# Kernel tuning notes

Hardware: AMD Instinct MI355X
Metric: run time of the kernel (lower is better)

Reference implementation:

```python
import jax, jax.numpy as jnp
import numpy as np

DIM = 1536
HEADS = 12
HEAD_DIM = 128
SEQ = 3120
FRAME = 1560
EPS = 1e-6


def _rmsnorm(x, gamma, eps=EPS):
    var = jnp.mean(jnp.square(x), axis=-1, keepdims=True)
    return x * jax.lax.rsqrt(var + eps) * gamma


def _rope(x, cos, sin):
    # x: [B,S,H,D], cos/sin: [S, D//2]; rotate interleaved pairs (Wan-style)
    xr = x.reshape(x.shape[:-1] + (x.shape[-1] // 2, 2))
    x1, x2 = xr[..., 0], xr[..., 1]
    c = cos[None, :, None, :]
    s = sin[None, :, None, :]
    o1 = x1 * c - x2 * s
    o2 = x1 * s + x2 * c
    return jnp.stack([o1, o2], axis=-1).reshape(x.shape)


def setup_inputs() -> dict:
    key = jax.random.key(0)
    ks = jax.random.split(key, 8)
    pos = jnp.arange(SEQ, dtype=jnp.float32)[:, None]
    inv_freq = 1.0 / (10000.0 ** (jnp.arange(0, HEAD_DIM // 2, dtype=jnp.float32) / (HEAD_DIM // 2)))
    ang = pos * inv_freq[None, :]
    return {
        "hidden_states": jax.random.normal(ks[0], (1, SEQ, DIM), jnp.float32),
        "freqs_cos": jnp.cos(ang),
        "freqs_sin": jnp.sin(ang),
        "w_qkv": jax.random.normal(ks[1], (DIM, 3 * DIM), jnp.float32) * (DIM ** -0.5),
        "b_qkv": jnp.zeros((3 * DIM,), jnp.float32),
        "g_q": jnp.ones((DIM,), jnp.float32),
        "g_k": jnp.ones((DIM,), jnp.float32),
        "w_out": jax.random.normal(ks[2], (DIM, DIM), jnp.float32) * (DIM ** -0.5),
        "b_out": jnp.zeros((DIM,), jnp.float32),
        "frame_len": FRAME,
    }


def reference(hidden_states, freqs_cos, freqs_sin, w_qkv, b_qkv, g_q, g_k, w_out, b_out, frame_len):
    B, S, _ = hidden_states.shape
    qkv = hidden_states @ w_qkv + b_qkv  # [B,S,3*DIM]
    q, k, v = jnp.split(qkv, 3, axis=-1)
    q = _rmsnorm(q, g_q)
    k = _rmsnorm(k, g_k)
    q = q.reshape(B, S, HEADS, HEAD_DIM)
    k = k.reshape(B, S, HEADS, HEAD_DIM)
    v = v.reshape(B, S, HEADS, HEAD_DIM)
    q = _rope(q, freqs_cos, freqs_sin)
    k = _rope(k, freqs_cos, freqs_sin)
    # block-wise causal mask over frames of frame_len tokens
    blk = jnp.arange(S) // frame_len
    mask = blk[None, :] <= blk[:, None]  # [Sq, Sk]
    scale = 1.0 / jnp.sqrt(jnp.float32(HEAD_DIM))
    scores = jnp.einsum("bqhd,bkhd->bhqk", q, k) * scale
    scores = jnp.where(mask[None, None], scores, jnp.float32(-1e30))
    probs = jax.nn.softmax(scores, axis=-1)
    out = jnp.einsum("bhqk,bkhd->bqhd", probs, v)
    out = out.reshape(B, S, HEADS * HEAD_DIM)
    return out @ w_out + b_out
```

## Files before the change

### kernel.cpp

```cpp
#include <hip/hip_runtime.h>
#include <hip/hip_bf16.h>
#include <stdint.h>

#define SEQ_LEN 3120
#define DIM 1536
#define QKV_N 4608
#define HEADS 12
#define HEAD_DIM 128
#define FRAME_LEN 1560
#define SM_SCALE 0.08838834764831845f
#define LOG2E 1.4426950408889634f
#define FMAXC2 43.280851226669165f
#define BQ 256

#if __has_builtin(__builtin_amdgcn_exp2f)
#define FEXP2(x) __builtin_amdgcn_exp2f(x)
#else
#define FEXP2(x) exp2f(x)
#endif

typedef short short8 __attribute__((ext_vector_type(8)));
typedef float f32x4 __attribute__((ext_vector_type(4)));
typedef float f32x16 __attribute__((ext_vector_type(16)));

__device__ __forceinline__ unsigned short f2bf(float x) {
    union { float f; unsigned u; } v; v.f = x;
    unsigned r = v.u + 0x7fffu + ((v.u >> 16) & 1u);
    return (unsigned short)(r >> 16);
}
__device__ __forceinline__ float bf2f(unsigned short b) {
    union { unsigned u; float f; } v; v.u = ((unsigned)b) << 16;
    return v.f;
}
__device__ __forceinline__ unsigned pk2bf(float a, float b) {
    __hip_bfloat162 h = __float22bfloat162_rn(make_float2(a, b));
    union { __hip_bfloat162 h2; unsigned u; } v; v.h2 = h;
    return v.u;
}

__device__ __forceinline__ void async16(void* lds, const void* g) {
    __builtin_amdgcn_global_load_lds(
        (const __attribute__((address_space(1))) unsigned int*)g,
        (__attribute__((address_space(3))) unsigned int*)lds, 16, 0, 0);
}

__device__ __forceinline__ void transpose_tile(
    const float* __restrict__ in, unsigned short* __restrict__ out,
    int R, int C, int c0, int r0, float (*T)[65], int tid)
{
    const int rl = tid >> 4, cl = (tid & 15) * 4;
#pragma unroll
    for (int i = 0; i < 4; ++i) {
        const int row = r0 + rl + i * 16;
        float4 v = *(const float4*)&in[(size_t)row * C + c0 + cl];
        T[cl + 0][rl + i * 16] = v.x; T[cl + 1][rl + i * 16] = v.y;
        T[cl + 2][rl + i * 16] = v.z; T[cl + 3][rl + i * 16] = v.w;
    }
    __syncthreads();
    const int oc = tid >> 2, ob = (tid & 3) * 16;
    union { unsigned short t[16]; uint4 u[2]; } p;
#pragma unroll
    for (int j = 0; j < 16; ++j) p.t[j] = f2bf(T[oc][ob + j]);
    uint4* dst = (uint4*)&out[(size_t)(c0 + oc) * R + r0 + ob];
    dst[0] = p.u[0];
    dst[1] = p.u[1];
}

__global__ __launch_bounds__(256) void prep_kernel(
    const float* __restrict__ hs, unsigned short* __restrict__ hsb,
    const float* __restrict__ w_qkv, unsigned short* __restrict__ wqkvT,
    const float* __restrict__ w_out, unsigned short* __restrict__ woutT)
{
    __shared__ float T[64][65];
    const int bid = blockIdx.x;
    const int tid = threadIdx.x;
    if (bid < 2340) {
        const int i = bid * 256 + tid;
        const float4 a = ((const float4*)hs)[i * 2];
        const float4 b = ((const float4*)hs)[i * 2 + 1];
        union { unsigned short t[8]; uint4 u; } p;
        p.t[0] = f2bf(a.x); p.t[1] = f2bf(a.y); p.t[2] = f2bf(a.z); p.t[3] = f2bf(a.w);
        p.t[4] = f2bf(b.x); p.t[5] = f2bf(b.y); p.t[6] = f2bf(b.z); p.t[7] = f2bf(b.w);
        ((uint4*)hsb)[i] = p.u;
    } else if (bid < 4068) {
        const int t = bid - 2340;
        transpose_tile(w_qkv, wqkvT, DIM, QKV_N, (t % 72) * 64, (t / 72) * 64, T, tid);
    } else {
        const int t = bid - 4068;
        transpose_tile(w_out, woutT, DIM, DIM, (t % 24) * 64, (t / 24) * 64, T, tid);
    }
}

__global__ __launch_bounds__(256, 2) void gemm_bt_kernel(
    const unsigned short* __restrict__ A, const unsigned short* __restrict__ Bt,
    const float* __restrict__ bias, float* __restrict__ C, int M, int N, int K,
    int ntp, int spx)
{
    __shared__ short As[2][4096];
    __shared__ short Bs[2][4096];

    const int xcd = blockIdx.x & 7;
    const int idx = (xcd & 1) * spx + (blockIdx.x >> 3);
    const int mtiles = (M + 127) >> 7;
    if (idx >= ntp * mtiles) return;
    const int m0 = (idx / ntp) * 128;
    const int n0 = ((xcd >> 1) * ntp + idx % ntp) * 128;

    const int tid = threadIdx.x;
    const int w = tid >> 6, l = tid & 63;
    const int wr = w >> 1, wc = w & 1;
    const int lhi = l >> 4, llo = l & 15;

    f32x4 acc[4][4];
#pragma unroll
    for (int i = 0; i < 4; ++i)
#pragma unroll
        for (int j = 0; j < 4; ++j) acc[i][j] = f32x4{0.f, 0.f, 0.f, 0.f};

    const int c0i = (w * 2) * 64 + l, c1i = c0i + 64;
    const unsigned short* gA0 = A + (size_t)min(m0 + (c0i >> 2), M - 1) * K + (c0i & 3) * 8;
    const unsigned short* gA1 = A + (size_t)min(m0 + (c1i >> 2), M - 1) * K + (c1i & 3) * 8;
    const unsigned short* gB0 = Bt + (size_t)(n0 + (c0i >> 2)) * K + (c0i & 3) * 8;
    const unsigned short* gB1 = Bt + (size_t)(n0 + (c1i >> 2)) * K + (c1i & 3) * 8;

    const int aoff = (wr * 64 + llo) * 32 + lhi * 8;
    const int boff = (wc * 64 + llo) * 32 + lhi * 8;

    auto stage = [&](int k0, int b) {
        async16(As[b] + (w * 2 + 0) * 512, gA0 + k0);
        async16(As[b] + (w * 2 + 1) * 512, gA1 + k0);
        async16(Bs[b] + (w * 2 + 0) * 512, gB0 + k0);
        async16(Bs[b] + (w * 2 + 1) * 512, gB1 + k0);
    };

    const int nk = K >> 5;
    stage(0, 0);
    for (int t = 0; t < nk; ++t) {
        __syncthreads();
        if (t + 1 < nk) stage((t + 1) * 32, (t + 1) & 1);
        const short* A_ = As[t & 1];
        const short* B_ = Bs[t & 1];
        short8 af[4], bf[4];
#pragma unroll
        for (int mt = 0; mt < 4; ++mt) af[mt] = *(const short8*)&A_[aoff + mt * 512];
#pragma unroll
        for (int nt = 0; nt < 4; ++nt) bf[nt] = *(const short8*)&B_[boff + nt * 512];
#pragma unroll
        for (int mt = 0; mt < 4; ++mt)
#pragma unroll
            for (int nt = 0; nt < 4; ++nt)
                acc[mt][nt] = __builtin_amdgcn_mfma_f32_16x16x32_bf16(af[mt], bf[nt], acc[mt][nt], 0, 0, 0);
    }

#pragma unroll
    for (int mt = 0; mt < 4; ++mt)
#pragma unroll
        for (int ri = 0; ri < 4; ++ri) {
            const int row = m0 + wr * 64 + mt * 16 + lhi * 4 + ri;
            if (row < M) {
#pragma unroll
                for (int nt = 0; nt < 4; ++nt) {
                    const int col = n0 + wc * 64 + nt * 16 + llo;
                    C[(size_t)row * N + col] = acc[mt][nt][ri] + bias[col];
                }
            }
        }
}

__global__ __launch_bounds__(256, 2) void gemm_bt_bf16_kernel(
    const unsigned short* __restrict__ A, const unsigned short* __restrict__ Bt,
    const float* __restrict__ bias, unsigned short* __restrict__ C, int M, int N, int K,
    int ntp, int spx)
{
    __shared__ short As[2][4096];
    __shared__ short Bs[2][4096];

    const int xcd = blockIdx.x & 7;
    const int idx = (xcd & 1) * spx + (blockIdx.x >> 3);
    const int mtiles = (M + 127) >> 7;
    if (idx >= ntp * mtiles) return;
    const int m0 = (idx / ntp) * 128;
    const int n0 = ((xcd >> 1) * ntp + idx % ntp) * 128;

    const int tid = threadIdx.x;
    const int w = tid >> 6, l = tid & 63;
    const int wr = w >> 1, wc = w & 1;
    const int lhi = l >> 4, llo = l & 15;

    f32x4 acc[4][4];
#pragma unroll
    for (int i = 0; i < 4; ++i)
#pragma unroll
        for (int j = 0; j < 4; ++j) acc[i][j] = f32x4{0.f, 0.f, 0.f, 0.f};

    const int c0i = (w * 2) * 64 + l, c1i = c0i + 64;
    const unsigned short* gA0 = A + (size_t)min(m0 + (c0i >> 2), M - 1) * K + (c0i & 3) * 8;
    const unsigned short* gA1 = A + (size_t)min(m0 + (c1i >> 2), M - 1) * K + (c1i & 3) * 8;
    const unsigned short* gB0 = Bt + (size_t)(n0 + (c0i >> 2)) * K + (c0i & 3) * 8;
    const unsigned short* gB1 = Bt + (size_t)(n0 + (c1i >> 2)) * K + (c1i & 3) * 8;

    const int aoff = (wr * 64 + llo) * 32 + lhi * 8;
    const int boff = (wc * 64 + llo) * 32 + lhi * 8;

    auto stage = [&](int k0, int b) {
        async16(As[b] + (w * 2 + 0) * 512, gA0 + k0);
        async16(As[b] + (w * 2 + 1) * 512, gA1 + k0);
        async16(Bs[b] + (w * 2 + 0) * 512, gB0 + k0);
        async16(Bs[b] + (w * 2 + 1) * 512, gB1 + k0);
    };

    const int nk = K >> 5;
    stage(0, 0);
    for (int t = 0; t < nk; ++t) {
        __syncthreads();
        if (t + 1 < nk) stage((t + 1) * 32, (t + 1) & 1);
        const short* A_ = As[t & 1];
        const short* B_ = Bs[t & 1];
        short8 af[4], bf[4];
#pragma unroll
        for (int mt = 0; mt < 4; ++mt) af[mt] = *(const short8*)&A_[aoff + mt * 512];
#pragma unroll
        for (int nt = 0; nt < 4; ++nt) bf[nt] = *(const short8*)&B_[boff + nt * 512];
#pragma unroll
        for (int mt = 0; mt < 4; ++mt)
#pragma unroll
            for (int nt = 0; nt < 4; ++nt)
                acc[mt][nt] = __builtin_amdgcn_mfma_f32_16x16x32_bf16(af[mt], bf[nt], acc[mt][nt], 0, 0, 0);
    }

#pragma unroll
    for (int mt = 0; mt < 4; ++mt)
#pragma unroll
        for (int ri = 0; ri < 4; ++ri) {
            const int row = m0 + wr * 64 + mt * 16 + lhi * 4 + ri;
            if (row < M) {
#pragma unroll
                for (int nt = 0; nt < 4; ++nt) {
                    const int col = n0 + wc * 64 + nt * 16 + llo;
                    C[(size_t)row * N + col] = f2bf(acc[mt][nt][ri] + bias[col]);
                }
            }
        }
}

__global__ __launch_bounds__(256) void rmsrope_kernel(
    const unsigned short* __restrict__ qkvb, const float* __restrict__ gq,
    const float* __restrict__ gk, const float* __restrict__ cosf,
    const float* __restrict__ sinf, unsigned short* __restrict__ qb,
    unsigned short* __restrict__ kb)
{
    const int s = blockIdx.x;
    const int tid = threadIdx.x;
    const unsigned short* qrow = qkvb + (size_t)s * QKV_N;
    const unsigned short* krow = qrow + DIM;

    float2 qp[3], kp[3];
    float ssq_q = 0.f, ssq_k = 0.f;
#pragma unroll
    for (int j = 0; j < 3; ++j) {
        const int p = tid + j * 256;
        const unsigned uq = *(const unsigned*)(qrow + 2 * p);
        const unsigned uk = *(const unsigned*)(krow + 2 * p);
        qp[j] = make_float2(bf2f((unsigned short)(uq & 0xffff)), bf2f((unsigned short)(uq >> 16)));
        kp[j] = make_float2(bf2f((unsigned short)(uk & 0xffff)), bf2f((unsigned short)(uk >> 16)));
        ssq_q += qp[j].x * qp[j].x + qp[j].y * qp[j].y;
        ssq_k += kp[j].x * kp[j].x + kp[j].y * kp[j].y;
    }
#pragma unroll
    for (int off = 32; off > 0; off >>= 1) {
        ssq_q += __shfl_down(ssq_q, off);
        ssq_k += __shfl_down(ssq_k, off);
    }
    __shared__ float wq[4], wk[4];
    const int wave = tid >> 6, lane = tid & 63;
    if (lane == 0) { wq[wave] = ssq_q; wk[wave] = ssq_k; }
    __syncthreads();
    const float tq = wq[0] + wq[1] + wq[2] + wq[3];
    const float tk = wk[0] + wk[1] + wk[2] + wk[3];
    const float inv_q = rsqrtf(tq * (1.0f / DIM) + 1e-6f) * (SM_SCALE * LOG2E);
    const float inv_k = rsqrtf(tk * (1.0f / DIM) + 1e-6f);

#pragma unroll
    for (int j = 0; j < 3; ++j) {
        const int p = tid + j * 256;
        const int fi = p & 63;
        const float c = cosf[s * 64 + fi];
        const float si = sinf[s * 64 + fi];
        {
            const float y1 = qp[j].x * inv_q * gq[2 * p];
            const float y2 = qp[j].y * inv_q * gq[2 * p + 1];
            *(unsigned*)&qb[(size_t)s * DIM + 2 * p] = pk2bf(y1 * c - y2 * si, y1 * si + y2 * c);
        }
        {
            const float y1 = kp[j].x * inv_k * gk[2 * p];
            const float y2 = kp[j].y * inv_k * gk[2 * p + 1];
            *(unsigned*)&kb[(size_t)s * DIM + 2 * p] = pk2bf(y1 * c - y2 * si, y1 * si + y2 * c);
        }
    }
}

__global__ __launch_bounds__(256) void vtrans_kernel(
    const unsigned short* __restrict__ qkvb, unsigned short* __restrict__ vt)
{
    __shared__ float T[128][65];
    const int s0 = blockIdx.x * 64;
    const int h = blockIdx.y;
    const int tid = threadIdx.x;
    const int rl = tid >> 2, cb = (tid & 3) * 32;
    const int row = min(s0 + rl, SEQ_LEN - 1);
#pragma unroll
    for (int i = 0; i < 4; ++i) {
        const int d = cb + i * 8;
        union { uint4 u; unsigned short t[8]; } v;
        v.u = *(const uint4*)&qkvb[(size_t)row * QKV_N + 2 * DIM + h * HEAD_DIM + d];
#pragma unroll
        for (int j = 0; j < 8; ++j) T[d + j][rl] = bf2f(v.t[j]);
    }
    __syncthreads();
    const int od = tid >> 1, ob = (tid & 1) * 32;
    const size_t orow = (size_t)(h * HEAD_DIM + od) * SEQ_LEN;
#pragma unroll
    for (int v8 = 0; v8 < 4; ++v8) {
        const int s = s0 + ob + v8 * 8;
        if (s < SEQ_LEN) {
            union { unsigned short t[8]; uint4 u; } pk;
#pragma unroll
            for (int j = 0; j < 8; ++j) pk.t[j] = f2bf(T[od][ob + v8 * 8 + j]);
            *(uint4*)&vt[orow + s] = pk.u;
        }
    }
}

__global__ __launch_bounds__(512, 2) void attn_part_kernel(
    const unsigned short* __restrict__ qb, const unsigned short* __restrict__ kb,
    const unsigned short* __restrict__ vt, unsigned short* __restrict__ part_o,
    float* __restrict__ part_ml)
{
    __shared__ short KV[40960];

    const int bid = blockIdx.x;
    const int xcd = bid & 7;
    const int slot = bid >> 3;
    int h, bx;
    if (slot < 20) { h = xcd; bx = slot; }
    else { h = 8 + (xcd >> 1); bx = (xcd & 1) * 10 + (slot - 20); }

    const int tid = threadIdx.x;
    const int w = tid >> 6;
    const int l = tid & 63;
    int tile, split, nsp;
    if (bx < 6) { tile = bx; split = 0; nsp = 1; }
    else { const int b2 = bx - 6; tile = 6 + (b2 >> 1); split = b2 & 1; nsp = 2; }
    const int q0 = tile * BQ;
    const int lhi = l >> 5;
    const int llo = l & 31;

#pragma unroll
    for (int s = 0; s < 8; ++s) {
        const int c = (s * 8 + w) * 64 + l;
        const int row = c >> 4, g = c & 15;
        const int gr = min(q0 + row, SEQ_LEN - 1);
        async16(KV + (s * 8 + w) * 512, qb + (size_t)gr * DIM + h * HEAD_DIM + g * 8);
    }
    __syncthreads();
    short8 qf[8];
#pragma unroll
    for (int ds = 0; ds < 8; ++ds)
        qf[ds] = *(const short8*)&KV[(w * 32 + llo) * 128 + ds * 16 + lhi * 8];
    __syncthreads();

    const int myq = q0 + w * 32 + llo;
    const int mylimit = (myq < FRAME_LEN) ? FRAME_LEN : SEQ_LEN;
    const int wave_lim = (q0 + w * 32 < FRAME_LEN) ? FRAME_LEN : SEQ_LEN;
    const int Lmax = (tile < 6) ? FRAME_LEN : SEQ_LEN;
    const int nch = (Lmax + 63) >> 6;
    const int kc0 = ((split * nch) / nsp) * 64;
    const int kc1 = (((split + 1) * nch) / nsp) * 64;
    const int nchunks = (kc1 - kc0) >> 6;

    float l_run = 0.f;
    f32x16 o[4];
#pragma unroll
    for (int mt = 0; mt < 4; ++mt)
#pragma unroll
        for (int r = 0; r < 16; ++r) o[mt][r] = 0.f;

    int krloc[2], kcol[2], vcol[2], lof[2];
    size_t vrow[2];
#pragma unroll
    for (int s = 0; s < 2; ++s) {
        const int c = (s * 8 + w) * 64 + l;
        const int kr = c >> 4;
        krloc[s] = kr;
        kcol[s] = h * HEAD_DIM + (((c & 15) ^ (kr & 7)) * 8);
        const int d = c >> 3;
        vrow[s] = (size_t)(h * HEAD_DIM + d) * SEQ_LEN;
        vcol[s] = ((c & 7) ^ (d & 7)) * 8;
        lof[s] = (s * 8 + w) * 512;
    }

    auto issueK = [&](int kc, int b) {
#pragma unroll
        for (int s = 0; s < 2; ++s) {
            const int gr = min(kc + krloc[s], SEQ_LEN - 1);
            async16(KV + b * 8192 + lof[s], kb + (size_t)gr * DIM + kcol[s]);
        }
    };
    auto issueV = [&](int kc, int t) {
#pragma unroll
        for (int s = 0; s < 2; ++s) {
            const int col = min(kc + vcol[s], SEQ_LEN - 8);
            async16(KV + 16384 + t * 8192 + lof[s], vt + vrow[s] + col);
        }
    };

    auto qkt = [&](f32x16* st, int b) {
        const short* Kb = KV + b * 8192;
#pragma unroll
        for (int r = 0; r < 16; ++r) { st[0][r] = 0.f; st[1][r] = 0.f; }
#pragma unroll
        for (int ds = 0; ds < 8; ++ds) {
            const int gd = ds * 2 + lhi;
#pragma unroll
            for (int kt = 0; kt < 2; ++kt) {
                const int krow = kt * 32 + llo;
                short8 kf = *(const short8*)&Kb[krow * 128 + ((gd ^ (krow & 7)) * 8)];
                st[kt] = __builtin_amdgcn_mfma_f32_32x32x16_bf16(kf, qf[ds], st[kt], 0, 0, 0);
            }
        }
    };

    auto sm_pv = [&](f32x16* st, int kc, int t) {
        if (kc + 64 > wave_lim) {
#pragma unroll
            for (int kt = 0; kt < 2; ++kt)
#pragma unroll
                for (int r = 0; r < 16; ++r) {
                    const int kg = kc + kt * 32 + (r & 3) + 8 * (r >> 2) + 4 * lhi;
                    if (kg >= mylimit) st[kt][r] = -3.0e38f;
                }
        }
        float rs = 0.f;
        unsigned p16[2][8];
#pragma unroll
        for (int kt = 0; kt < 2; ++kt)
#pragma unroll
            for (int r2 = 0; r2 < 8; ++r2) {
                const float p0 = FEXP2(st[kt][2 * r2] - FMAXC2);
                const float p1 = FEXP2(st[kt][2 * r2 + 1] - FMAXC2);
                rs += p0 + p1;
                p16[kt][r2] = pk2bf(p0, p1);
            }
        l_run += rs;

        const short* Vb = KV + 16384 + t * 8192;
#pragma unroll
        for (int kblk = 0; kblk < 4; ++kblk) {
            const int tt = kblk >> 1;
            const int i0 = (kblk & 1) * 4;
            union { unsigned u[4]; short8 s8; } pf;
#if __has_builtin(__builtin_amdgcn_permlane32_swap)
            {
                auto s02 = __builtin_amdgcn_permlane32_swap(
                    p16[tt][i0 + 0], p16[tt][i0 + 2], false, false);
                auto s13 = __builtin_amdgcn_permlane32_swap(
                    p16[tt][i0 + 1], p16[tt][i0 + 3], false, false);
                pf.u[0] = s02[0]; pf.u[1] = s13[0];
                pf.u[2] = s02[1]; pf.u[3] = s13[1];
            }
#else
            {
                const int dk    = ((kblk & 1) * 2 + lhi) * 2;
                const int dsend = ((kblk & 1) * 2 + (1 - lhi)) * 2;
                const unsigned r0 = __shfl_xor(p16[tt][dsend], 32);
                const unsigned r1 = __shfl_xor(p16[tt][dsend + 1], 32);
                if (lhi == 0) { pf.u[0] = p16[tt][dk]; pf.u[1] = p16[tt][dk + 1]; pf.u[2] = r0; pf.u[3] = r1; }
                else          { pf.u[0] = r0; pf.u[1] = r1; pf.u[2] = p16[tt][dk]; pf.u[3] = p16[tt][dk + 1]; }
            }
#endif
#pragma unroll
            for (int mt = 0; mt < 4; ++mt) {
                const int vd = mt * 32 + llo;
                short8 vf = *(const short8*)&Vb[vd * 64 + (((kblk * 2 + lhi) ^ (vd & 7)) * 8)];
                o[mt] = __builtin_amdgcn_mfma_f32_32x32x16_bf16(vf, pf.s8, o[mt], 0, 0, 0);
            }
        }
    };

    issueK(kc0, 0); issueV(kc0, 0);
    if (nchunks > 1) { issueK(kc0 + 64, 1); issueV(kc0 + 64, 1); }
    __syncthreads();
    f32x16 stC[2];
    qkt(stC, 0);

    int vcur = 0;
    for (int i = 0, kc = kc0; i < nchunks; ++i, kc += 64) {
        __syncthreads();
        if (i + 2 < nchunks) {
            issueK(kc + 128, i & 1);
            int vt2 = vcur + 2; if (vt2 >= 3) vt2 -= 3;
            issueV(kc + 128, vt2);
        }
        f32x16 stN[2];
        if (i + 1 < nchunks) qkt(stN, (i + 1) & 1);
        sm_pv(stC, kc, vcur);
        if (i + 1 < nchunks) { stC[0] = stN[0]; stC[1] = stN[1]; }
        vcur = (vcur == 2) ? 0 : vcur + 1;
    }

    const float l_tot = l_run + __shfl_xor(l_run, 32);
    const int slot_o = bx * HEADS + h;
    const int qloc = w * 32 + llo;
    const float inv = (l_tot > 0.f) ? 1.0f / l_tot : 0.f;
    unsigned short* op = part_o + (size_t)slot_o * (BQ * HEAD_DIM) + qloc * HEAD_DIM + 4 * lhi;
#pragma unroll
    for (int mt = 0; mt < 4; ++mt)
#pragma unroll
        for (int g = 0; g < 4; ++g) {
            uint2 u;
            u.x = pk2bf(o[mt][4 * g + 0] * inv, o[mt][4 * g + 1] * inv);
            u.y = pk2bf(o[mt][4 * g + 2] * inv, o[mt][4 * g + 3] * inv);
            *(uint2*)&op[mt * 32 + 8 * g] = u;
        }
    if (lhi == 0) part_ml[(size_t)slot_o * BQ + qloc] = l_tot;
}

__global__ __launch_bounds__(256) void attn_combine_kernel(
    const unsigned short* __restrict__ part_o, const float* __restrict__ part_ml,
    unsigned short* __restrict__ attb)
{
    const int h = blockIdx.y;
    const int q = blockIdx.x * 8 + (threadIdx.x >> 5);
    const int dq = (threadIdx.x & 31) * 4;
    const int tile = q >> 8, qloc = q & 255;
    int base_bx, ns;
    if (tile < 6) { base_bx = tile; ns = 1; }
    else { base_bx = 6 + (tile - 6) * 2; ns = 2; }

    float W = 0.f;
    float acc[4] = {0.f, 0.f, 0.f, 0.f};
    for (int s = 0; s < ns; ++s) {
        const int slot = (base_bx + s) * HEADS + h;
        const float w = part_ml[(size_t)slot * BQ + qloc];
        if (w > 0.f) {
            W += w;
            const unsigned short* po = part_o +
                (size_t)slot * (BQ * HEAD_DIM) + qloc * HEAD_DIM + dq;
            uint2 u = *(const uint2*)po;
            acc[0] += w * bf2f((unsigned short)(u.x & 0xffff));
            acc[1] += w * bf2f((unsigned short)(u.x >> 16));
            acc[2] += w * bf2f((unsigned short)(u.y & 0xffff));
            acc[3] += w * bf2f((unsigned short)(u.y >> 16));
        }
    }
    const float inv = 1.0f / W;
    uint2 pk;
    pk.x = pk2bf(acc[0] * inv, acc[1] * inv);
    pk.y = pk2bf(acc[2] * inv, acc[3] * inv);
    *(uint2*)&attb[(size_t)q * DIM + h * HEAD_DIM + dq] = pk;
}

extern "C" void kernel_launch(void* const* d_in, const int* in_sizes, int n_in,
                              void* d_out, int out_size, void* d_ws, size_t ws_size,
                              hipStream_t stream)
{
    const float* hs    = (const float*)d_in[0];
    const float* cosf  = (const float*)d_in[1];
    const float* sinf  = (const float*)d_in[2];
    const float* w_qkv = (const float*)d_in[3];
    const float* b_qkv = (const float*)d_in[4];
    const float* g_q   = (const float*)d_in[5];
    const float* g_k   = (const float*)d_in[6];
    const float* w_out = (const float*)d_in[7];
    const float* b_out = (const float*)d_in[8];

    char* base = (char*)d_ws;
    unsigned short* qb     = (unsigned short*)base;
    unsigned short* kb     = (unsigned short*)(base + 9584640);
    unsigned short* vt     = (unsigned short*)(base + 19169280);
    unsigned short* hsb    = vt;
    unsigned short* qkvb   = (unsigned short*)(base + 28753920);
    unsigned short* part_o = (unsigned short*)(base + 28753920);
    float*          part_ml= (float*)(base + 60211200);
    unsigned short* wqkvT  = (unsigned short*)(base + 81469440);
    unsigned short* attb   = wqkvT;
    unsigned short* woutT  = (unsigned short*)(base + 95625216);
    float* outp = (float*)d_out;

    prep_kernel<<<4644, 256, 0, stream>>>(hs, hsb, w_qkv, wqkvT, w_out, woutT);
    gemm_bt_bf16_kernel<<<904, 256, 0, stream>>>(
        hsb, wqkvT, b_qkv, qkvb, SEQ_LEN, QKV_N, DIM, 9, 113);
    rmsrope_kernel<<<SEQ_LEN, 256, 0, stream>>>(qkvb, g_q, g_k, cosf, sinf, qb, kb);
    vtrans_kernel<<<dim3((SEQ_LEN + 63) / 64, HEADS), 256, 0, stream>>>(qkvb, vt);
    attn_part_kernel<<<240, 512, 0, stream>>>(qb, kb, vt, part_o, part_ml);
    attn_combine_kernel<<<dim3(SEQ_LEN / 8, HEADS), 256, 0, stream>>>(part_o, part_ml, attb);
    gemm_bt_kernel<<<304, 256, 0, stream>>>(
        attb, woutT, b_out, outp, SEQ_LEN, DIM, DIM, 3, 38);
}
```

Baseline: 296.4 us.

## Replace QKV GEMM with 256x256-tile, 512-thread kernel using swizzled LDS

Replaces the 128x128 QKV projection GEMM with a 256x256 output tile computed by 8 waves, a K-step of 64 and a 128 KB double-buffered LDS layout whose 16-byte chunks are XOR-swizzled to avoid bank conflicts. Workgroups are assigned to XCDs in contiguous chunks, and MFMA sections are wrapped in s_setprio. The aim is more data reuse per LDS load and less global traffic. The cost is only 234 workgroups on a 256-CU part, some M padding waste, and high register pressure from 32 accumulators per thread.

Result: faster. 284.6 us (-4.0%).

```diff
diff --git a/kernel.cpp b/kernel.cpp
--- a/kernel.cpp
+++ b/kernel.cpp
@@ -167,77 +167,104 @@
         }
 }
 
-__global__ __launch_bounds__(256, 2) void gemm_bt_bf16_kernel(
+__global__ __launch_bounds__(512, 2) void gemm256_bf16_kernel(
     const unsigned short* __restrict__ A, const unsigned short* __restrict__ Bt,
-    const float* __restrict__ bias, unsigned short* __restrict__ C, int M, int N, int K,
-    int ntp, int spx)
-{
-    __shared__ short As[2][4096];
-    __shared__ short Bs[2][4096];
-
+    const float* __restrict__ bias, unsigned short* __restrict__ C,
+    int M, int N, int K)
+{
+    __shared__ short LDS[65536];
+
+    const int mtiles = (M + 255) >> 8;
+    const int nwg = mtiles * (N >> 8);
+    const int q = nwg >> 3, r = nwg & 7;
     const int xcd = blockIdx.x & 7;
-    const int idx = (xcd & 1) * spx + (blockIdx.x >> 3);
-    const int mtiles = (M + 127) >> 7;
-    if (idx >= ntp * mtiles) return;
-    const int m0 = (idx / ntp) * 128;
-    const int n0 = ((xcd >> 1) * ntp + idx % ntp) * 128;
+    const int g0 = (xcd < r) ? xcd * (q + 1) : r * (q + 1) + (xcd - r) * q;
+    const int g = g0 + (int)(blockIdx.x >> 3);
+    const int m0 = (g % mtiles) * 256;
+    const int n0 = (g / mtiles) * 256;
 
     const int tid = threadIdx.x;
     const int w = tid >> 6, l = tid & 63;
-    const int wr = w >> 1, wc = w & 1;
+    const int wr = w >> 2, wc = w & 3;
     const int lhi = l >> 4, llo = l & 15;
 
-    f32x4 acc[4][4];
-#pragma unroll
-    for (int i = 0; i < 4; ++i)
+    f32x4 acc[8][4];
+#pragma unroll
+    for (int i = 0; i < 8; ++i)
 #pragma unroll
         for (int j = 0; j < 4; ++j) acc[i][j] = f32x4{0.f, 0.f, 0.f, 0.f};
 
-    const int c0i = (w * 2) * 64 + l, c1i = c0i + 64;
-    const unsigned short* gA0 = A + (size_t)min(m0 + (c0i >> 2), M - 1) * K + (c0i & 3) * 8;
-    const unsigned short* gA1 = A + (size_t)min(m0 + (c1i >> 2), M - 1) * K + (c1i & 3) * 8;
-    const unsigned short* gB0 = Bt + (size_t)(n0 + (c0i >> 2)) * K + (c0i & 3) * 8;
-    const unsigned short* gB1 = Bt + (size_t)(n0 + (c1i >> 2)) * K + (c1i & 3) * 8;
-
-    const int aoff = (wr * 64 + llo) * 32 + lhi * 8;
-    const int boff = (wc * 64 + llo) * 32 + lhi * 8;
-
-    auto stage = [&](int k0, int b) {
-        async16(As[b] + (w * 2 + 0) * 512, gA0 + k0);
-        async16(As[b] + (w * 2 + 1) * 512, gA1 + k0);
-        async16(Bs[b] + (w * 2 + 0) * 512, gB0 + k0);
-        async16(Bs[b] + (w * 2 + 1) * 512, gB1 + k0);
+    const unsigned short* gsrc[8];
+#pragma unroll
+    for (int j = 0; j < 4; ++j) {
+        const int c = (j * 8 + w) * 64 + l;
+        const int row = c >> 3, ks = c & 7;
+        gsrc[j] = A + (size_t)min(m0 + row, M - 1) * K + (ks ^ (row & 7)) * 8;
+    }
+#pragma unroll
+    for (int j = 0; j < 4; ++j) {
+        const int c = (j * 8 + w) * 64 + l;
+        const int row = c >> 3, ks = c & 7;
+        gsrc[4 + j] = Bt + (size_t)min(n0 + row, N - 1) * K + (ks ^ (row & 7)) * 8;
+    }
+
+    auto stageAll = [&](int kt, int b) {
+        short* dst = LDS + b * 32768;
+#pragma unroll
+        for (int j = 0; j < 4; ++j)
+            async16(dst + (j * 8 + w) * 512, gsrc[j] + kt * 64);
+#pragma unroll
+        for (int j = 0; j < 4; ++j)
+            async16(dst + 16384 + (j * 8 + w) * 512, gsrc[4 + j] + kt * 64);
     };
 
-    const int nk = K >> 5;
-    stage(0, 0);
+    const int nk = K >> 6;
+    stageAll(0, 0);
+    asm volatile("s_waitcnt vmcnt(0)\n\ts_barrier" ::: "memory");
+
     for (int t = 0; t < nk; ++t) {
-        __syncthreads();
-        if (t + 1 < nk) stage((t + 1) * 32, (t + 1) & 1);
-        const short* A_ = As[t & 1];
-        const short* B_ = Bs[t & 1];
-        short8 af[4], bf[4];
-#pragma unroll
-        for (int mt = 0; mt < 4; ++mt) af[mt] = *(const short8*)&A_[aoff + mt * 512];
-#pragma unroll
-        for (int nt = 0; nt < 4; ++nt) bf[nt] = *(const short8*)&B_[boff + nt * 512];
-#pragma unroll
-        for (int mt = 0; mt < 4; ++mt)
-#pragma unroll
-            for (int nt = 0; nt < 4; ++nt)
-                acc[mt][nt] = __builtin_amdgcn_mfma_f32_16x16x32_bf16(af[mt], bf[nt], acc[mt][nt], 0, 0, 0);
-    }
-
-#pragma unroll
-    for (int mt = 0; mt < 4; ++mt)
+        if (t + 1 < nk) stageAll(t + 1, (t + 1) & 1);
+        const short* Ab = LDS + (t & 1) * 32768;
+        const short* Bb = Ab + 16384;
+#pragma unroll
+        for (int ph = 0; ph < 2; ++ph) {
+            short8 bfr[4];
+#pragma unroll
+            for (int nt = 0; nt < 4; ++nt) {
+                const int rb = wc * 64 + nt * 16 + llo;
+                bfr[nt] = *(const short8*)&Bb[rb * 64 + ((ph * 4 + lhi) ^ (rb & 7)) * 8];
+            }
+#pragma unroll
+            for (int mh = 0; mh < 2; ++mh) {
+                short8 afr[4];
+#pragma unroll
+                for (int mt = 0; mt < 4; ++mt) {
+                    const int ra = wr * 128 + mh * 64 + mt * 16 + llo;
+                    afr[mt] = *(const short8*)&Ab[ra * 64 + ((ph * 4 + lhi) ^ (ra & 7)) * 8];
+                }
+                __builtin_amdgcn_s_setprio(1);
+#pragma unroll
+                for (int mt = 0; mt < 4; ++mt)
+#pragma unroll
+                    for (int nt = 0; nt < 4; ++nt)
+                        acc[mh * 4 + mt][nt] = __builtin_amdgcn_mfma_f32_16x16x32_bf16(
+                            afr[mt], bfr[nt], acc[mh * 4 + mt][nt], 0, 0, 0);
+                __builtin_amdgcn_s_setprio(0);
+            }
+        }
+        asm volatile("s_waitcnt vmcnt(0)\n\ts_barrier" ::: "memory");
+    }
+
+#pragma unroll
+    for (int mi = 0; mi < 8; ++mi)
 #pragma unroll
         for (int ri = 0; ri < 4; ++ri) {
-            const int row = m0 + wr * 64 + mt * 16 + lhi * 4 + ri;
+            const int row = m0 + wr * 128 + mi * 16 + lhi * 4 + ri;
             if (row < M) {
 #pragma unroll
                 for (int nt = 0; nt < 4; ++nt) {
                     const int col = n0 + wc * 64 + nt * 16 + llo;
-                    C[(size_t)row * N + col] = f2bf(acc[mt][nt][ri] + bias[col]);
+                    C[(size_t)row * N + col] = f2bf(acc[mi][nt][ri] + bias[col]);
                 }
             }
         }
@@ -588,8 +615,8 @@
     float* outp = (float*)d_out;
 
     prep_kernel<<<4644, 256, 0, stream>>>(hs, hsb, w_qkv, wqkvT, w_out, woutT);
-    gemm_bt_bf16_kernel<<<904, 256, 0, stream>>>(
-        hsb, wqkvT, b_qkv, qkvb, SEQ_LEN, QKV_N, DIM, 9, 113);
+    gemm256_bf16_kernel<<<234, 512, 0, stream>>>(
+        hsb, wqkvT, b_qkv, qkvb, SEQ_LEN, QKV_N, DIM);
     rmsrope_kernel<<<SEQ_LEN, 256, 0, stream>>>(qkvb, g_q, g_k, cosf, sinf, qb, kb);
     vtrans_kernel<<<dim3((SEQ_LEN + 63) / 64, HEADS), 256, 0, stream>>>(qkvb, vt);
     attn_part_kernel<<<240, 512, 0, stream>>>(qb, kb, vt, part_o, part_ml);
```
